# Kernel optimization log

Measured on AMD Instinct MI355X. Metric: run time of the kernel, lower is better.

## Reference

```python
import jax, jax.numpy as jnp
import numpy as np

HID = 512
J = 64
NEG = -1e9


def _gru_cell(x, h, Wih, Whh, bih, bhh):
    # PyTorch GRUCell: gates stacked as (r, z, n) along first dim of (3H, in)
    gi = Wih @ x + bih          # (3H,)
    gh = Whh @ h + bhh          # (3H,)
    r = jax.nn.sigmoid(gi[:HID] + gh[:HID])
    z = jax.nn.sigmoid(gi[HID:2 * HID] + gh[HID:2 * HID])
    n = jnp.tanh(gi[2 * HID:] + r * gh[2 * HID:])
    return (1.0 - z) * n + z * h


def setup_inputs() -> dict:
    key = jax.random.key(0)
    ks = jax.random.split(key, 8)
    T = 4096
    state_dim = 2 * J  # input is state[t][1:]
    d = {
        "state": jax.random.normal(ks[0], (T, state_dim + 1), dtype=jnp.float32),
        "h_prev": jnp.zeros((2, HID), dtype=jnp.float32),
        "mask": jax.random.randint(ks[1], (J, J), 0, 2, dtype=jnp.int32),
        "Wih0": jax.random.normal(ks[2], (3 * HID, state_dim), dtype=jnp.float32) * 0.05,
        "Whh0": jax.random.normal(ks[3], (3 * HID, HID), dtype=jnp.float32) * 0.04,
        "bih0": jnp.zeros((3 * HID,), dtype=jnp.float32),
        "bhh0": jnp.zeros((3 * HID,), dtype=jnp.float32),
        "Wih1": jax.random.normal(ks[4], (3 * HID, HID), dtype=jnp.float32) * 0.04,
        "Whh1": jax.random.normal(ks[5], (3 * HID, HID), dtype=jnp.float32) * 0.04,
        "bih1": jnp.zeros((3 * HID,), dtype=jnp.float32),
        "bhh1": jnp.zeros((3 * HID,), dtype=jnp.float32),
        "Wfc": jax.random.normal(ks[6], (J * J, HID), dtype=jnp.float32) * 0.06,
        "bfc": jnp.zeros((J * J,), dtype=jnp.float32),
    }
    return d


def reference(state, h_prev, mask, Wih0, Whh0, bih0, bhh0,
              Wih1, Whh1, bih1, bhh1, Wfc, bfc):
    xs = state[:, 1:]  # drop leading element, matches state[t][1:]

    def step(hs, x_t):
        h0 = _gru_cell(x_t, hs[0], Wih0, Whh0, bih0, bhh0)
        h1 = _gru_cell(h0, hs[1], Wih1, Whh1, bih1, bhh1)
        new = jnp.stack([h0, h1])
        return new, h1

    h_next, h_list = jax.lax.scan(step, h_prev, xs)  # h_list: (T, HID)
    logits = jax.nn.relu(h_list @ Wfc.T + bfc)       # (T, J*J)
    logits = logits.reshape(-1, J, J)
    logits = jnp.where(mask == 0, jnp.float32(NEG), logits)
    return logits, h_next
```

## Files before the change

kernel.cpp:

```cpp
#include <hip/hip_runtime.h>
#include <stdint.h>

#define TS 4096
#define NEG_VAL -1000000000.0f

typedef _Float16 h2 __attribute__((ext_vector_type(2)));
typedef unsigned long long u64t;

#define GI0_OFF   ((size_t)0)
#define H1_OFF    ((size_t)25165824)
#define MB0L0_OFF ((size_t)33554432)
#define MB0L1_OFF ((size_t)33816576)
#define MB1L1_OFF ((size_t)34340864)
#define PROGS_OFF ((size_t)34865152)
#define PROGH_OFF ((size_t)34867200)
#define TICK_OFF  ((size_t)34867712)
#define WS_NEED   ((size_t)34867776)

static __device__ __forceinline__ u64t ld_a64(const u64t* p){
  return __hip_atomic_load(p, __ATOMIC_RELAXED, __HIP_MEMORY_SCOPE_AGENT);
}
static __device__ __forceinline__ void st_a64(u64t* p, u64t v){
  __hip_atomic_store(p, v, __ATOMIC_RELAXED, __HIP_MEMORY_SCOPE_AGENT);
}
static __device__ __forceinline__ unsigned ld_u32(const unsigned* p){
  return __hip_atomic_load(p, __ATOMIC_RELAXED, __HIP_MEMORY_SCOPE_AGENT);
}
static __device__ __forceinline__ void st_u32(unsigned* p, unsigned v){
  __hip_atomic_store(p, v, __ATOMIC_RELAXED, __HIP_MEMORY_SCOPE_AGENT);
}
static __device__ __forceinline__ float sigmoidf_(float x){
  return 1.0f / (1.0f + __expf(-x));
}
static __device__ __forceinline__ float tanhf_(float x){
  float ax = fabsf(x);
  float e  = __expf(-2.0f*ax);
  float t  = (1.0f - e) / (1.0f + e);
  return copysignf(t, x);
}
static __device__ __forceinline__ uint32_t pack2h(float a, float b){
  _Float16 ha = (_Float16)a, hb = (_Float16)b;
  unsigned short ua = __builtin_bit_cast(unsigned short, ha);
  unsigned short ub = __builtin_bit_cast(unsigned short, hb);
  return (uint32_t)ua | ((uint32_t)ub << 16);
}
static __device__ __forceinline__ h2 u2h2(uint32_t u){ return __builtin_bit_cast(h2, u); }
static __device__ __forceinline__ unsigned tg(u64t v){ return (unsigned)(v>>32); }

template<int CTRL>
static __device__ __forceinline__ float dppx(float x){
  return __int_as_float(__builtin_amdgcn_update_dpp(0, __float_as_int(x), CTRL, 0xF, 0xF, true));
}
static __device__ __forceinline__ float qsum8(float x){
  x += dppx<0xB1>(x);
  x += dppx<0x4E>(x);
  x += __shfl_xor(x, 4, 64);
  return x;
}
static __device__ __forceinline__ float qsum16(float x){
  x += dppx<0xB1>(x);
  x += dppx<0x4E>(x);
  x += __shfl_xor(x, 4, 64);
  x += __shfl_xor(x, 8, 64);
  return x;
}
static __device__ __forceinline__ int wave_min(int v){
  #pragma unroll
  for (int off=32; off; off>>=1){ int o = __shfl_xor(v, off, 64); v = o<v?o:v; }
  return v;
}

#if __has_builtin(__builtin_amdgcn_fdot2)
#define FDOT2(a,b,c) __builtin_amdgcn_fdot2((a),(b),(c),false)
#else
static __device__ __forceinline__ float FDOT2(h2 a, h2 b, float c){
  return c + (float)a[0]*(float)b[0] + (float)a[1]*(float)b[1];
}
#endif

static __device__ __forceinline__ void poll4(const u64t* base, unsigned want,
                                             uint32_t (&v)[4], long* bd, bool* fail){
  u64t p0=ld_a64(base), p1=ld_a64(base+1), p2=ld_a64(base+2), p3=ld_a64(base+3);
  for(;;){
    bool ok = (tg(p0)==want)&&(tg(p1)==want)&&(tg(p2)==want)&&(tg(p3)==want);
    if (__all(ok)) break;
    if (--(*bd) < 0){ *fail = true; break; }
    __builtin_amdgcn_s_sleep(1);
    if (tg(p0)!=want) p0=ld_a64(base);
    if (tg(p1)!=want) p1=ld_a64(base+1);
    if (tg(p2)!=want) p2=ld_a64(base+2);
    if (tg(p3)!=want) p3=ld_a64(base+3);
  }
  v[0]=(uint32_t)p0; v[1]=(uint32_t)p1; v[2]=(uint32_t)p2; v[3]=(uint32_t)p3;
}
static __device__ __forceinline__ void seg32(h2* dst, const float* src){
  const float4* p = (const float4*)src;
  #pragma unroll
  for (int k=0;k<16;++k){
    float4 v = p[k];
    dst[2*k]   = h2{(_Float16)v.x,(_Float16)v.y};
    dst[2*k+1] = h2{(_Float16)v.z,(_Float16)v.w};
  }
}
static __device__ __forceinline__ void seg16(h2* dst, const float* src){
  const float4* p = (const float4*)src;
  #pragma unroll
  for (int k=0;k<8;++k){
    float4 v = p[k];
    dst[2*k]   = h2{(_Float16)v.x,(_Float16)v.y};
    dst[2*k+1] = h2{(_Float16)v.z,(_Float16)v.w};
  }
}

__global__ __launch_bounds__(512,1) void actor_fused(
    const float* __restrict__ hprev,
    const int*   __restrict__ mask,
    const float* __restrict__ Whh0,
    const float* __restrict__ bhh0,
    const float* __restrict__ Wih1,
    const float* __restrict__ Whh1,
    const float* __restrict__ bih1,
    const float* __restrict__ bhh1,
    const float* __restrict__ Wfc,
    const float* __restrict__ bfc,
    const float* __restrict__ gi0,
    float* __restrict__ H1,
    u64t* mb0l0, u64t* mb0l1, u64t* mb1l1,
    unsigned* progS, unsigned* progH, unsigned* ticket,
    float* __restrict__ out, float* __restrict__ hnext)
{
  const int wg   = blockIdx.x;
  const int tid  = threadIdx.x;
  const int wv   = tid >> 6;
  const int lane = tid & 63;
  __shared__ __align__(16) float lds[6464];
  volatile int* fcp = (volatile int*)lds;
  long bd = 1L<<22;
  bool fail = false;

  if (wg < 24){
    if (wg < 8){
      const int j = lane & 7;
      const int o = wg*64 + (tid>>3);
      h2 w[96];
      seg32(&w[0],  Whh0 + (size_t)o*512         + 64*j);
      seg32(&w[32], Whh0 + (size_t)(512+o)*512   + 64*j);
      seg32(&w[64], Whh0 + (size_t)(1024+o)*512  + 64*j);
      const float br=bhh0[o], bz=bhh0[512+o], bn=bhh0[1024+o];
      float hreg = hprev[o];
      if ((tid&1)==0)
        st_a64(mb0l0 + ((size_t)wg*16 + 15)*256 + (tid>>1),
               ((u64t)1<<32) | pack2h(hprev[tid], hprev[tid+1]));
      if (tid==0) fcp[0] = 0;
      __syncthreads();

      for (int t=0; t<TS; ++t){
        if ((t&3)==0){
          if (wv==0 && lane==0) st_u32(progS + wg*16, (unsigned)(t-1));
          if (t>=16){
            const int need = t-11;
            if (wv==0){
              int v = (lane<24)? (int)ld_u32(progS + lane*16) : 0x7fffffff;
              int mn = wave_min(v);
              while (mn < need){
                if (--bd<0){ fail=true; break; }
                __builtin_amdgcn_s_sleep(4);
                v = (lane<24)? (int)ld_u32(progS + lane*16) : 0x7fffffff;
                mn = wave_min(v);
              }
              if (lane==0) fcp[0] = t;
            } else {
              while (fcp[0] < t){ if (--bd<0){ fail=true; break; } __builtin_amdgcn_s_sleep(4); }
            }
            if (fail) break;
          }
        }
        const float* gp = gi0 + (size_t)t*1536;
        const float gr = gp[o], gz = gp[512+o], gn = gp[1024+o];

        uint32_t v[4];
        poll4(mb0l0 + ((size_t)wg*16 + ((t-1)&15))*256 + 4*lane, (unsigned)(t+1), v, &bd, &fail);
        if (fail) break;
        uint32_t hw[32];
        const int sj = 8*j;
        #pragma unroll
        for (int i=0;i<8;++i){
          const int src = sj + i;
          hw[4*i+0] = (uint32_t)__shfl((int)v[0], src, 64);
          hw[4*i+1] = (uint32_t)__shfl((int)v[1], src, 64);
          hw[4*i+2] = (uint32_t)__shfl((int)v[2], src, 64);
          hw[4*i+3] = (uint32_t)__shfl((int)v[3], src, 64);
        }
        float a0=0.f, a1=0.f, a2=0.f;
        #pragma unroll
        for (int m=0;m<32;++m){
          h2 hv = u2h2(hw[m]);
          a0 = FDOT2(w[m],    hv, a0);
          a1 = FDOT2(w[32+m], hv, a1);
          a2 = FDOT2(w[64+m], hv, a2);
        }
        a0 = qsum8(a0); a1 = qsum8(a1); a2 = qsum8(a2);

        const float r = sigmoidf_(gr + a0 + br);
        const float z = sigmoidf_(gz + a1 + bz);
        const float n = tanhf_(gn + r*(a2 + bn));
        const float h = (1.f - z)*n + z*hreg;
        hreg = h;

        const float hx = __shfl_xor(h, 8, 64);
        const uint32_t wval = (o&1)? pack2h(hx,h) : pack2h(h,hx);
        const u64t word = ((u64t)(unsigned)(t+2)<<32) | wval;
        const int wi = wg*32 + (tid>>4);
        const int d = (tid&7) | (((tid>>3)&1)<<3);
        const int slot = t&15;
        if (d<8){
          st_a64(mb0l0 + ((size_t)d*16 + slot)*256 + wi, word);
          st_a64(mb0l1 + ((size_t)(8+d)*16 + slot)*256 + wi, word);
        } else {
          st_a64(mb0l1 + ((size_t)(d-8)*16 + slot)*256 + wi, word);
        }
        if (t==TS-1 && j==0) hnext[o] = h;
      }
    } else {
      const int q = wg-8;
      const int j = lane & 15;
      const int ol = q*32 + (tid>>4);
      h2 w[96];
      seg16(&w[0],  Whh1 + (size_t)ol*512         + 32*j);
      seg16(&w[16], Whh1 + (size_t)(512+ol)*512   + 32*j);
      seg16(&w[32], Whh1 + (size_t)(1024+ol)*512  + 32*j);
      seg16(&w[48], Wih1 + (size_t)ol*512         + 32*j);
      seg16(&w[64], Wih1 + (size_t)(512+ol)*512   + 32*j);
      seg16(&w[80], Wih1 + (size_t)(1024+ol)*512  + 32*j);
      const float brc = bih1[ol]      + bhh1[ol];
      const float bzc = bih1[512+ol]  + bhh1[512+ol];
      const float bin = bih1[1024+ol];
      const float bhn = bhh1[1024+ol];
      float hreg = hprev[512+ol];
      if ((tid&1)==0)
        st_a64(mb1l1 + ((size_t)q*16 + 15)*256 + (tid>>1),
               ((u64t)1<<32) | pack2h(hprev[512+tid], hprev[512+tid+1]));
      if (tid==0) fcp[0] = 0;
      __syncthreads();

      for (int s=0; s<TS; ++s){
        if ((s&3)==0){
          if (wv==0 && lane==0) st_u32(progS + wg*16, (unsigned)(s-1));
          if (s>=16){
            const int need = s-11;
            if (wv==0){
              int v = (lane<24)? (int)ld_u32(progS + lane*16) : 0x7fffffff;
              int mn = wave_min(v);
              while (mn < need){
                if (--bd<0){ fail=true; break; }
                __builtin_amdgcn_s_sleep(4);
                v = (lane<24)? (int)ld_u32(progS + lane*16) : 0x7fffffff;
                mn = wave_min(v);
              }
              if (lane==0) fcp[0] = s;
            } else {
              while (fcp[0] < s){ if (--bd<0){ fail=true; break; } __builtin_amdgcn_s_sleep(4); }
            }
            if (fail) break;
          }
        }
        uint32_t va[4], vb[4];
        poll4(mb1l1 + ((size_t)q*16 + ((s-1)&15))*256 + 4*lane, (unsigned)(s+1), va, &bd, &fail);
        if (fail) break;
        poll4(mb0l1 + ((size_t)q*16 + (s&15))*256 + 4*lane, (unsigned)(s+2), vb, &bd, &fail);
        if (fail) break;
        uint32_t h1w[16], h0w[16];
        const int s4 = 4*j;
        #pragma unroll
        for (int rr=0;rr<4;++rr){
          const int src = s4 + rr;
          h1w[4*rr+0]=(uint32_t)__shfl((int)va[0],src,64);
          h1w[4*rr+1]=(uint32_t)__shfl((int)va[1],src,64);
          h1w[4*rr+2]=(uint32_t)__shfl((int)va[2],src,64);
          h1w[4*rr+3]=(uint32_t)__shfl((int)va[3],src,64);
          h0w[4*rr+0]=(uint32_t)__shfl((int)vb[0],src,64);
          h0w[4*rr+1]=(uint32_t)__shfl((int)vb[1],src,64);
          h0w[4*rr+2]=(uint32_t)__shfl((int)vb[2],src,64);
          h0w[4*rr+3]=(uint32_t)__shfl((int)vb[3],src,64);
        }
        float a0=0.f,a1=0.f,a2=0.f,b0=0.f,b1=0.f,b2=0.f;
        #pragma unroll
        for (int m=0;m<16;++m){
          h2 hv1 = u2h2(h1w[m]);
          h2 hv0 = u2h2(h0w[m]);
          a0 = FDOT2(w[m],    hv1, a0);
          a1 = FDOT2(w[16+m], hv1, a1);
          a2 = FDOT2(w[32+m], hv1, a2);
          b0 = FDOT2(w[48+m], hv0, b0);
          b1 = FDOT2(w[64+m], hv0, b1);
          b2 = FDOT2(w[80+m], hv0, b2);
        }
        const float sr  = qsum16(a0+b0);
        const float sz  = qsum16(a1+b1);
        const float shn = qsum16(a2);
        const float sin_= qsum16(b2);

        const float r = sigmoidf_(sr + brc);
        const float z = sigmoidf_(sz + bzc);
        const float n = tanhf_((sin_ + bin) + r*(shn + bhn));
        const float h = (1.f - z)*n + z*hreg;
        hreg = h;

        if (j==0) H1[(size_t)s*512 + ol] = h;
        const float hx = __shfl_xor(h, 16, 64);
        const uint32_t wval = (ol&1)? pack2h(hx,h) : pack2h(h,hx);
        const u64t word = ((u64t)(unsigned)(s+2)<<32) | wval;
        const int wi = q*16 + (tid>>5);
        const int d = (tid&15) | (((tid>>4)&1)<<4);
        if (d<16)
          st_a64(mb1l1 + ((size_t)d*16 + (s&15))*256 + wi, word);
        if ((s&15)==15 && lane==0)
          __hip_atomic_store(progH + q*8 + wv, (unsigned)(s+1),
                             __ATOMIC_RELEASE, __HIP_MEMORY_SCOPE_AGENT);
        if (s==TS-1 && j==0) hnext[512+ol] = h;
      }
      if (lane==0)
        __hip_atomic_store(progH + q*8 + wv, (unsigned)TS,
                           __ATOMIC_RELEASE, __HIP_MEMORY_SCOPE_AGENT);
    }
  } else {
    float* As = lds;
    float* Bs = lds + 32*132;
    int*   comm = (int*)&lds[6460];
    const int tm = tid>>4, tn = tid&15;
    const int m0 = tid>>2, kk0a = (tid&3)*8;
    const int n0 = tid>>3, kk0b = (tid&7)*4;
    long fcbd = 1L<<24;
    for(;;){
      if (tid==0) comm[0] = (int)atomicAdd(ticket, 1u);
      __syncthreads();
      const int tau = comm[0];
      __syncthreads();
      if (tau >= 2048) break;
      const int bm = tau>>6, bn = tau&63;
      if (tid==0){
        const unsigned need = (unsigned)(bm*128 + 128);
        for(;;){
          unsigned mn = 0xffffffffu;
          for (int k2=0;k2<128;++k2){ unsigned v = ld_u32(progH+k2); mn = v<mn?v:mn; }
          if (mn >= need) break;
          __builtin_amdgcn_s_sleep(16);
          if (--fcbd < 0) break;
        }
      }
      __syncthreads();
      __builtin_amdgcn_fence(__ATOMIC_ACQUIRE, "agent");

      const float* A = H1  + (size_t)bm*128*512;
      const float* B = Wfc + (size_t)bn*64*512;
      float acc[4][4] = {};
      for (int k0=0; k0<512; k0+=32){
        #pragma unroll
        for (int jj=0;jj<8;++jj) As[(kk0a+jj)*132 + m0] = A[(size_t)m0*512 + k0+kk0a+jj];
        #pragma unroll
        for (int jj=0;jj<4;++jj) Bs[(kk0b+jj)*68  + n0] = B[(size_t)n0*512 + k0+kk0b+jj];
        __syncthreads();
        #pragma unroll
        for (int kk=0;kk<32;++kk){
          const float4 av = *(const float4*)&As[kk*132 + tm*4];
          const float4 bv = *(const float4*)&Bs[kk*68  + tn*4];
          acc[0][0]=fmaf(av.x,bv.x,acc[0][0]); acc[0][1]=fmaf(av.x,bv.y,acc[0][1]);
          acc[0][2]=fmaf(av.x,bv.z,acc[0][2]); acc[0][3]=fmaf(av.x,bv.w,acc[0][3]);
          acc[1][0]=fmaf(av.y,bv.x,acc[1][0]); acc[1][1]=fmaf(av.y,bv.y,acc[1][1]);
          acc[1][2]=fmaf(av.y,bv.z,acc[1][2]); acc[1][3]=fmaf(av.y,bv.w,acc[1][3]);
          acc[2][0]=fmaf(av.z,bv.x,acc[2][0]); acc[2][1]=fmaf(av.z,bv.y,acc[2][1]);
          acc[2][2]=fmaf(av.z,bv.z,acc[2][2]); acc[2][3]=fmaf(av.z,bv.w,acc[2][3]);
          acc[3][0]=fmaf(av.w,bv.x,acc[3][0]); acc[3][1]=fmaf(av.w,bv.y,acc[3][1]);
          acc[3][2]=fmaf(av.w,bv.z,acc[3][2]); acc[3][3]=fmaf(av.w,bv.w,acc[3][3]);
        }
        __syncthreads();
      }
      const int cc0 = bn*64 + tn*4;
      const int mk0 = mask[cc0], mk1 = mask[cc0+1], mk2 = mask[cc0+2], mk3 = mask[cc0+3];
      const float b0 = bfc[cc0], b1 = bfc[cc0+1], b2 = bfc[cc0+2], b3 = bfc[cc0+3];
      #pragma unroll
      for (int i=0;i<4;++i){
        const int mm = bm*128 + tm*4 + i;
        float4 vv;
        vv.x = fmaxf(acc[i][0]+b0, 0.f); if (mk0==0) vv.x = NEG_VAL;
        vv.y = fmaxf(acc[i][1]+b1, 0.f); if (mk1==0) vv.y = NEG_VAL;
        vv.z = fmaxf(acc[i][2]+b2, 0.f); if (mk2==0) vv.z = NEG_VAL;
        vv.w = fmaxf(acc[i][3]+b3, 0.f); if (mk3==0) vv.w = NEG_VAL;
        *(float4*)&out[(size_t)mm*4096 + cc0] = vv;
      }
    }
  }
}

__global__ __launch_bounds__(256) void gemm_gi0(
    const float* __restrict__ A, int lda,
    const float* __restrict__ B, int ldb,
    float* __restrict__ C, int ldc,
    const float* __restrict__ bias, int K)
{
  __shared__ __align__(16) float As[32][68];
  __shared__ __align__(16) float Bs[32][68];
  const int bm = blockIdx.y*64, bn = blockIdx.x*64;
  const int tid = threadIdx.x;
  const int tm = tid>>4, tn = tid&15;
  float acc[4][4] = {};
  const int m0 = tid>>2, kk0 = (tid&3)*8;
  for (int k0=0; k0<K; k0+=32){
    #pragma unroll
    for (int j=0;j<8;++j) As[kk0+j][m0] = A[(size_t)(bm+m0)*lda + k0+kk0+j];
    #pragma unroll
    for (int j=0;j<8;++j) Bs[kk0+j][m0] = B[(size_t)(bn+m0)*ldb + k0+kk0+j];
    __syncthreads();
    #pragma unroll
    for (int kk=0;kk<32;++kk){
      const float4 av = *(const float4*)&As[kk][tm*4];
      const float4 bv = *(const float4*)&Bs[kk][tn*4];
      acc[0][0]=fmaf(av.x,bv.x,acc[0][0]); acc[0][1]=fmaf(av.x,bv.y,acc[0][1]);
      acc[0][2]=fmaf(av.x,bv.z,acc[0][2]); acc[0][3]=fmaf(av.x,bv.w,acc[0][3]);
      acc[1][0]=fmaf(av.y,bv.x,acc[1][0]); acc[1][1]=fmaf(av.y,bv.y,acc[1][1]);
      acc[1][2]=fmaf(av.y,bv.z,acc[1][2]); acc[1][3]=fmaf(av.y,bv.w,acc[1][3]);
      acc[2][0]=fmaf(av.z,bv.x,acc[2][0]); acc[2][1]=fmaf(av.z,bv.y,acc[2][1]);
      acc[2][2]=fmaf(av.z,bv.z,acc[2][2]); acc[2][3]=fmaf(av.z,bv.w,acc[2][3]);
      acc[3][0]=fmaf(av.w,bv.x,acc[3][0]); acc[3][1]=fmaf(av.w,bv.y,acc[3][1]);
      acc[3][2]=fmaf(av.w,bv.z,acc[3][2]); acc[3][3]=fmaf(av.w,bv.w,acc[3][3]);
    }
    __syncthreads();
  }
  #pragma unroll
  for (int i=0;i<4;++i){
    #pragma unroll
    for (int j=0;j<4;++j){
      const int mm = bm + tm*4 + i, cc = bn + tn*4 + j;
      C[(size_t)mm*ldc + cc] = acc[i][j] + bias[cc];
    }
  }
}

extern "C" void kernel_launch(void* const* d_in, const int* in_sizes, int n_in,
                              void* d_out, int out_size, void* d_ws, size_t ws_size,
                              hipStream_t stream)
{
  const float* state = (const float*)d_in[0];
  const float* hprev = (const float*)d_in[1];
  const int*   mask  = (const int*)d_in[2];
  const float* Wih0  = (const float*)d_in[3];
  const float* Whh0  = (const float*)d_in[4];
  const float* bih0  = (const float*)d_in[5];
  const float* bhh0  = (const float*)d_in[6];
  const float* Wih1  = (const float*)d_in[7];
  const float* Whh1  = (const float*)d_in[8];
  const float* bih1  = (const float*)d_in[9];
  const float* bhh1  = (const float*)d_in[10];
  const float* Wfc   = (const float*)d_in[11];
  const float* bfc   = (const float*)d_in[12];

  if (ws_size < WS_NEED) return;

  float* out = (float*)d_out;
  char*  ws  = (char*)d_ws;
  float* gi0 = (float*)(ws + GI0_OFF);
  float* H1  = (float*)(ws + H1_OFF);
  u64t*  mb0l0 = (u64t*)(ws + MB0L0_OFF);
  u64t*  mb0l1 = (u64t*)(ws + MB0L1_OFF);
  u64t*  mb1l1 = (u64t*)(ws + MB1L1_OFF);
  unsigned* progS = (unsigned*)(ws + PROGS_OFF);
  unsigned* progH = (unsigned*)(ws + PROGH_OFF);
  unsigned* tick  = (unsigned*)(ws + TICK_OFF);

  (void)hipMemsetAsync(ws + MB0L0_OFF, 0, (size_t)(WS_NEED - MB0L0_OFF), stream);

  {
    dim3 grid(1536/64, 4096/64);
    gemm_gi0<<<grid, 256, 0, stream>>>(state+1, 129, Wih0, 128, gi0, 1536, bih0, 128);
  }

  actor_fused<<<256, 512, 0, stream>>>(
      hprev, mask, Whh0, bhh0, Wih1, Whh1, bih1, bhh1, Wfc, bfc,
      gi0, H1, mb0l0, mb0l1, mb1l1, progS, progH, tick,
      out, out + (size_t)4096*4096);
}
```

Baseline: 15.58 ms.

## Restructure GRU scan sync: LDS-staged mailbox polling, spread scan blocks, fp16 gi0

Rewrites the persistent GRU scan in the fused kernel. A single wave polls the inter-block mailboxes and stages the hidden-state words in LDS for the other waves, replacing the per-wave cross-lane shuffles. Scan blocks are spread across every eighth block index, mailbox depth goes from 16 to 32 slots, and progress checks run less often. The input-gate GEMM now writes fp16 output to halve its memory traffic and adds rounding error. The extra LDS flag handshakes may add latency on each step of the serial recurrence.

```diff
diff --git a/kernel.cpp b/kernel.cpp
--- a/kernel.cpp
+++ b/kernel.cpp
@@ -4,18 +4,19 @@
 #define TS 4096
 #define NEG_VAL -1000000000.0f
 
-typedef _Float16 h2 __attribute__((ext_vector_type(2)));
+typedef _Float16 h2    __attribute__((ext_vector_type(2)));
+typedef _Float16 f16x8 __attribute__((ext_vector_type(8)));
 typedef unsigned long long u64t;
 
-#define GI0_OFF   ((size_t)0)
-#define H1_OFF    ((size_t)25165824)
-#define MB0L0_OFF ((size_t)33554432)
-#define MB0L1_OFF ((size_t)33816576)
-#define MB1L1_OFF ((size_t)34340864)
-#define PROGS_OFF ((size_t)34865152)
-#define PROGH_OFF ((size_t)34867200)
-#define TICK_OFF  ((size_t)34867712)
-#define WS_NEED   ((size_t)34867776)
+#define GI0H_OFF  ((size_t)0)
+#define H1_OFF    ((size_t)12582912)
+#define MB0L0_OFF ((size_t)20971520)
+#define MB0L1_OFF ((size_t)21495808)
+#define MB1L1_OFF ((size_t)22544384)
+#define PROGS_OFF ((size_t)23592960)
+#define PROGH_OFF ((size_t)23594496)
+#define TICK_OFF  ((size_t)23594752)
+#define WS_NEED   ((size_t)23594816)
 
 static __device__ __forceinline__ u64t ld_a64(const u64t* p){
   return __hip_atomic_load(p, __ATOMIC_RELAXED, __HIP_MEMORY_SCOPE_AGENT);
@@ -52,16 +53,11 @@
   return __int_as_float(__builtin_amdgcn_update_dpp(0, __float_as_int(x), CTRL, 0xF, 0xF, true));
 }
 static __device__ __forceinline__ float qsum8(float x){
-  x += dppx<0xB1>(x);
-  x += dppx<0x4E>(x);
-  x += __shfl_xor(x, 4, 64);
+  x += dppx<0xB1>(x); x += dppx<0x4E>(x); x += __shfl_xor(x, 4, 64);
   return x;
 }
 static __device__ __forceinline__ float qsum16(float x){
-  x += dppx<0xB1>(x);
-  x += dppx<0x4E>(x);
-  x += __shfl_xor(x, 4, 64);
-  x += __shfl_xor(x, 8, 64);
+  x += dppx<0xB1>(x); x += dppx<0x4E>(x); x += __shfl_xor(x, 4, 64); x += __shfl_xor(x, 8, 64);
   return x;
 }
 static __device__ __forceinline__ int wave_min(int v){
@@ -71,46 +67,34 @@
 }
 
 #if __has_builtin(__builtin_amdgcn_fdot2)
-#define FDOT2(a,b,c) __builtin_amdgcn_fdot2((a),(b),(c),false)
+static __device__ __forceinline__ float FDOT2(h2 a, h2 b, float c){
+  return __builtin_amdgcn_fdot2(a, b, c, false);
+}
 #else
 static __device__ __forceinline__ float FDOT2(h2 a, h2 b, float c){
   return c + (float)a[0]*(float)b[0] + (float)a[1]*(float)b[1];
 }
 #endif
 
-static __device__ __forceinline__ void poll4(const u64t* base, unsigned want,
-                                             uint32_t (&v)[4], long* bd, bool* fail){
-  u64t p0=ld_a64(base), p1=ld_a64(base+1), p2=ld_a64(base+2), p3=ld_a64(base+3);
-  for(;;){
-    bool ok = (tg(p0)==want)&&(tg(p1)==want)&&(tg(p2)==want)&&(tg(p3)==want);
-    if (__all(ok)) break;
-    if (--(*bd) < 0){ *fail = true; break; }
-    __builtin_amdgcn_s_sleep(1);
-    if (tg(p0)!=want) p0=ld_a64(base);
-    if (tg(p1)!=want) p1=ld_a64(base+1);
-    if (tg(p2)!=want) p2=ld_a64(base+2);
-    if (tg(p3)!=want) p3=ld_a64(base+3);
-  }
-  v[0]=(uint32_t)p0; v[1]=(uint32_t)p1; v[2]=(uint32_t)p2; v[3]=(uint32_t)p3;
-}
-static __device__ __forceinline__ void seg32(h2* dst, const float* src){
-  const float4* p = (const float4*)src;
-  #pragma unroll
-  for (int k=0;k<16;++k){
-    float4 v = p[k];
-    dst[2*k]   = h2{(_Float16)v.x,(_Float16)v.y};
-    dst[2*k+1] = h2{(_Float16)v.z,(_Float16)v.w};
-  }
-}
-static __device__ __forceinline__ void seg16(h2* dst, const float* src){
-  const float4* p = (const float4*)src;
-  #pragma unroll
-  for (int k=0;k<8;++k){
-    float4 v = p[k];
-    dst[2*k]   = h2{(_Float16)v.x,(_Float16)v.y};
-    dst[2*k+1] = h2{(_Float16)v.z,(_Float16)v.w};
-  }
-}
+static __device__ __forceinline__ float dot8(f16x8 wv, const uint32_t* hw, float acc){
+  acc = FDOT2(h2{wv[0],wv[1]}, u2h2(hw[0]), acc);
+  acc = FDOT2(h2{wv[2],wv[3]}, u2h2(hw[1]), acc);
+  acc = FDOT2(h2{wv[4],wv[5]}, u2h2(hw[2]), acc);
+  acc = FDOT2(h2{wv[6],wv[7]}, u2h2(hw[3]), acc);
+  return acc;
+}
+
+#define DECL8(P) f16x8 P##0,P##1,P##2,P##3,P##4,P##5,P##6,P##7;
+#define DECL4(P) f16x8 P##0,P##1,P##2,P##3;
+#define LDW8(DST, PTR) { float4 _a=((const float4*)(PTR))[0]; float4 _b=((const float4*)(PTR))[1]; \
+  DST = f16x8{(_Float16)_a.x,(_Float16)_a.y,(_Float16)_a.z,(_Float16)_a.w, \
+              (_Float16)_b.x,(_Float16)_b.y,(_Float16)_b.z,(_Float16)_b.w}; }
+#define LOADROW8(P, BASE) LDW8(P##0,(BASE)) LDW8(P##1,(BASE)+8) LDW8(P##2,(BASE)+16) LDW8(P##3,(BASE)+24) \
+                          LDW8(P##4,(BASE)+32) LDW8(P##5,(BASE)+40) LDW8(P##6,(BASE)+48) LDW8(P##7,(BASE)+56)
+#define LOADROW4(P, BASE) LDW8(P##0,(BASE)) LDW8(P##1,(BASE)+8) LDW8(P##2,(BASE)+16) LDW8(P##3,(BASE)+24)
+#define DOT8x8(ACC,P,HW) ACC=dot8(P##0,(HW)+0,ACC);ACC=dot8(P##1,(HW)+4,ACC);ACC=dot8(P##2,(HW)+8,ACC);ACC=dot8(P##3,(HW)+12,ACC); \
+                         ACC=dot8(P##4,(HW)+16,ACC);ACC=dot8(P##5,(HW)+20,ACC);ACC=dot8(P##6,(HW)+24,ACC);ACC=dot8(P##7,(HW)+28,ACC);
+#define DOT8x4(ACC,P,HW) ACC=dot8(P##0,(HW)+0,ACC);ACC=dot8(P##1,(HW)+4,ACC);ACC=dot8(P##2,(HW)+8,ACC);ACC=dot8(P##3,(HW)+12,ACC);
 
 __global__ __launch_bounds__(512,1) void actor_fused(
     const float* __restrict__ hprev,
@@ -123,210 +107,298 @@
     const float* __restrict__ bhh1,
     const float* __restrict__ Wfc,
     const float* __restrict__ bfc,
-    const float* __restrict__ gi0,
+    const uint32_t* __restrict__ gi0h,
     float* __restrict__ H1,
     u64t* mb0l0, u64t* mb0l1, u64t* mb1l1,
     unsigned* progS, unsigned* progH, unsigned* ticket,
     float* __restrict__ out, float* __restrict__ hnext)
 {
-  const int wg   = blockIdx.x;
+  const int bx   = blockIdx.x;
   const int tid  = threadIdx.x;
   const int wv   = tid >> 6;
   const int lane = tid & 63;
-  __shared__ __align__(16) float lds[6464];
-  volatile int* fcp = (volatile int*)lds;
+  const bool isScan = ((bx & 7) == 0) && (bx < 192);
+  const int role = bx >> 3;
+
+  __shared__ __align__(16) uint32_t smem[6784];
   long bd = 1L<<22;
   bool fail = false;
 
-  if (wg < 24){
-    if (wg < 8){
-      const int j = lane & 7;
-      const int o = wg*64 + (tid>>3);
-      h2 w[96];
-      seg32(&w[0],  Whh0 + (size_t)o*512         + 64*j);
-      seg32(&w[32], Whh0 + (size_t)(512+o)*512   + 64*j);
-      seg32(&w[64], Whh0 + (size_t)(1024+o)*512  + 64*j);
-      const float br=bhh0[o], bz=bhh0[512+o], bn=bhh0[1024+o];
-      float hreg = hprev[o];
-      if ((tid&1)==0)
-        st_a64(mb0l0 + ((size_t)wg*16 + 15)*256 + (tid>>1),
-               ((u64t)1<<32) | pack2h(hprev[tid], hprev[tid+1]));
-      if (tid==0) fcp[0] = 0;
-      __syncthreads();
-
-      for (int t=0; t<TS; ++t){
-        if ((t&3)==0){
-          if (wv==0 && lane==0) st_u32(progS + wg*16, (unsigned)(t-1));
-          if (t>=16){
-            const int need = t-11;
-            if (wv==0){
-              int v = (lane<24)? (int)ld_u32(progS + lane*16) : 0x7fffffff;
-              int mn = wave_min(v);
-              while (mn < need){
-                if (--bd<0){ fail=true; break; }
-                __builtin_amdgcn_s_sleep(4);
-                v = (lane<24)? (int)ld_u32(progS + lane*16) : 0x7fffffff;
-                mn = wave_min(v);
-              }
-              if (lane==0) fcp[0] = t;
-            } else {
-              while (fcp[0] < t){ if (--bd<0){ fail=true; break; } __builtin_amdgcn_s_sleep(4); }
-            }
-            if (fail) break;
+  if (isScan && role < 8){
+    const int o = role*64 + (tid>>3);
+    const int j = tid&7;
+    DECL8(Ar) DECL8(Az) DECL8(An)
+    LOADROW8(Ar, Whh0 + (size_t)o*512         + 64*j)
+    LOADROW8(Az, Whh0 + (size_t)(512+o)*512   + 64*j)
+    LOADROW8(An, Whh0 + (size_t)(1024+o)*512  + 64*j)
+    const float br=bhh0[o], bz=bhh0[512+o], bn=bhh0[1024+o];
+    float hreg = hprev[o];
+    u64t* mbme = mb0l0 + (size_t)role*32*256;
+    volatile int* flg = (volatile int*)(smem+600);
+    volatile int* fcp = (volatile int*)(smem+604);
+    if ((tid&1)==0)
+      st_a64(mbme + (size_t)31*256 + (tid>>1), ((u64t)1<<32) | pack2h(hprev[tid], hprev[tid+1]));
+    if (tid==0){ flg[0]=-1; flg[1]=-1; fcp[0]=-1; }
+    __syncthreads();
+    u64t p0=0,p1=0,p2=0,p3=0;
+    if (wv==0){
+      const u64t* b = mbme + (size_t)31*256 + 4*lane;
+      p0=ld_a64(b); p1=ld_a64(b+1); p2=ld_a64(b+2); p3=ld_a64(b+3);
+    }
+
+    for (int t=0; t<TS; ++t){
+      if ((t&3)==0 && wv==2 && lane==0) st_u32(progS + role*16, (unsigned)t);
+      if ((t&15)==8 && t>=32){
+        if (wv==2){
+          const int need = t-10;
+          int v = (lane<24)? (int)ld_u32(progS + lane*16) : 0x7fffffff;
+          int mn = wave_min(v);
+          while (mn < need){
+            if (--bd<0){ fail=true; break; }
+            __builtin_amdgcn_s_sleep(8);
+            v = (lane<24)? (int)ld_u32(progS + lane*16) : 0x7fffffff;
+            mn = wave_min(v);
           }
-        }
-        const float* gp = gi0 + (size_t)t*1536;
-        const float gr = gp[o], gz = gp[512+o], gn = gp[1024+o];
-
-        uint32_t v[4];
-        poll4(mb0l0 + ((size_t)wg*16 + ((t-1)&15))*256 + 4*lane, (unsigned)(t+1), v, &bd, &fail);
+          if (lane==0) fcp[0] = t;
+        } else {
+          int c=0;
+          while (fcp[0] < t){ if(++c>(1<<20)){fail=true;break;} __builtin_amdgcn_s_sleep(4); }
+        }
         if (fail) break;
-        uint32_t hw[32];
-        const int sj = 8*j;
+      }
+      const uint32_t* gp = gi0h + (size_t)t*768 + (o>>1);
+      const uint32_t ga=gp[0], gb=gp[256], gc=gp[512];
+
+      if (wv==0){
+        const unsigned want = (unsigned)(t+1);
+        const u64t* b = mbme + (size_t)((t-1)&31)*256 + 4*lane;
+        int it=0;
+        for(;;){
+          bool ok = (tg(p0)==want)&&(tg(p1)==want)&&(tg(p2)==want)&&(tg(p3)==want);
+          if (__all(ok)) break;
+          if (--bd<0){ fail=true; break; }
+          if (++it>16) __builtin_amdgcn_s_sleep(2);
+          if (tg(p0)!=want) p0=ld_a64(b);
+          if (tg(p1)!=want) p1=ld_a64(b+1);
+          if (tg(p2)!=want) p2=ld_a64(b+2);
+          if (tg(p3)!=want) p3=ld_a64(b+3);
+        }
+        uint32_t* dst = smem + (t&1)*288 + 4*lane + 4*(lane>>3);
+        dst[0]=(uint32_t)p0; dst[1]=(uint32_t)p1; dst[2]=(uint32_t)p2; dst[3]=(uint32_t)p3;
+        asm volatile("s_waitcnt lgkmcnt(0)" ::: "memory");
+        if (fail){ flg[0]=0x7fffffff; flg[1]=0x7fffffff; break; }
+        if (lane==0) flg[t&1] = t;
+      }
+      { int c=0, fv;
+        while ((fv=flg[t&1]) != t){
+          if (fv>=0x40000000){ fail=true; break; }
+          if (++c>(1<<20)){ fail=true; break; }
+          __builtin_amdgcn_s_sleep(1);
+        }
+        if (fail) break;
+      }
+      asm volatile("" ::: "memory");
+      uint32_t hw[32];
+      { const uint32_t* src = smem + (t&1)*288 + 36*j;
         #pragma unroll
-        for (int i=0;i<8;++i){
-          const int src = sj + i;
-          hw[4*i+0] = (uint32_t)__shfl((int)v[0], src, 64);
-          hw[4*i+1] = (uint32_t)__shfl((int)v[1], src, 64);
-          hw[4*i+2] = (uint32_t)__shfl((int)v[2], src, 64);
-          hw[4*i+3] = (uint32_t)__shfl((int)v[3], src, 64);
-        }
-        float a0=0.f, a1=0.f, a2=0.f;
+        for (int k2=0;k2<8;++k2){
+          uint4 u = *(const uint4*)(src + 4*k2);
+          hw[4*k2]=u.x; hw[4*k2+1]=u.y; hw[4*k2+2]=u.z; hw[4*k2+3]=u.w;
+        } }
+      float a0=0.f,a1=0.f,a2=0.f;
+      DOT8x8(a0,Ar,hw) DOT8x8(a1,Az,hw) DOT8x8(a2,An,hw)
+      a0=qsum8(a0); a1=qsum8(a1); a2=qsum8(a2);
+
+      h2 g0=u2h2(ga), g1=u2h2(gb), g2=u2h2(gc);
+      const int half = o&1;
+      const float gr = half? (float)g0[1] : (float)g0[0];
+      const float gz = half? (float)g1[1] : (float)g1[0];
+      const float gn = half? (float)g2[1] : (float)g2[0];
+
+      const float r = sigmoidf_(gr + a0 + br);
+      const float z = sigmoidf_(gz + a1 + bz);
+      const float n = tanhf_(gn + r*(a2 + bn));
+      const float h = (1.f - z)*n + z*hreg;
+      hreg = h;
+
+      const float hx = __shfl_xor(h, 8, 64);
+      const uint32_t wval = half? pack2h(hx,h) : pack2h(h,hx);
+      const u64t word = ((u64t)(unsigned)(t+2)<<32) | wval;
+      const int wi = role*32 + (tid>>4);
+      const int d = (tid&7) | (((tid>>3)&1)<<3);
+      const int slot = t&31;
+      if (d<8){
+        st_a64(mb0l0 + ((size_t)d*32 + slot)*256 + wi, word);
+        st_a64(mb0l1 + ((size_t)(8+d)*32 + slot)*256 + wi, word);
+      } else {
+        st_a64(mb0l1 + ((size_t)(d-8)*32 + slot)*256 + wi, word);
+      }
+      if (t==TS-1 && j==0) hnext[o] = h;
+      if (wv==0){
+        const u64t* b = mbme + (size_t)(t&31)*256 + 4*lane;
+        p0=ld_a64(b); p1=ld_a64(b+1); p2=ld_a64(b+2); p3=ld_a64(b+3);
+      }
+    }
+  } else if (isScan){
+    const int q = role-8;
+    const int ol = q*32 + (tid>>4);
+    const int j = lane&15;
+    DECL4(Hr) DECL4(Hz) DECL4(Hn) DECL4(Ir) DECL4(Iz) DECL4(In)
+    LOADROW4(Hr, Whh1 + (size_t)ol*512         + 32*j)
+    LOADROW4(Hz, Whh1 + (size_t)(512+ol)*512   + 32*j)
+    LOADROW4(Hn, Whh1 + (size_t)(1024+ol)*512  + 32*j)
+    LOADROW4(Ir, Wih1 + (size_t)ol*512         + 32*j)
+    LOADROW4(Iz, Wih1 + (size_t)(512+ol)*512   + 32*j)
+    LOADROW4(In, Wih1 + (size_t)(1024+ol)*512  + 32*j)
+    const float brc = bih1[ol] + bhh1[ol];
+    const float bzc = bih1[512+ol] + bhh1[512+ol];
+    const float bin = bih1[1024+ol];
+    const float bhn = bhh1[1024+ol];
+    float hreg = hprev[512+ol];
+    u64t* mb1me = mb1l1 + (size_t)q*32*256;
+    u64t* mb0me = mb0l1 + (size_t)q*32*256;
+    volatile int* flgA = (volatile int*)(smem+1160);
+    volatile int* flgB = (volatile int*)(smem+1162);
+    volatile int* fcp  = (volatile int*)(smem+1166);
+    if ((tid&1)==0)
+      st_a64(mb1me + (size_t)31*256 + (tid>>1), ((u64t)1<<32) | pack2h(hprev[512+tid], hprev[512+tid+1]));
+    if (tid==0){ flgA[0]=-1; flgA[1]=-1; flgB[0]=-1; flgB[1]=-1; fcp[0]=-1; }
+    __syncthreads();
+    u64t pa0=0,pa1=0,pa2=0,pa3=0, pb0=0,pb1=0,pb2=0,pb3=0;
+    if (wv==0){
+      const u64t* b = mb1me + (size_t)31*256 + 4*lane;
+      pa0=ld_a64(b); pa1=ld_a64(b+1); pa2=ld_a64(b+2); pa3=ld_a64(b+3);
+    } else if (wv==1){
+      const u64t* b = mb0me + 4*lane;
+      pb0=ld_a64(b); pb1=ld_a64(b+1); pb2=ld_a64(b+2); pb3=ld_a64(b+3);
+    }
+
+    for (int s=0; s<TS; ++s){
+      if ((s&3)==0 && wv==2 && lane==32) st_u32(progS + role*16, (unsigned)s);
+      if ((s&15)==8 && s>=32){
+        if (wv==2){
+          const int need = s-10;
+          int v = (lane<16)? (int)ld_u32(progS + (8+lane)*16) : 0x7fffffff;
+          int mn = wave_min(v);
+          while (mn < need){
+            if (--bd<0){ fail=true; break; }
+            __builtin_amdgcn_s_sleep(8);
+            v = (lane<16)? (int)ld_u32(progS + (8+lane)*16) : 0x7fffffff;
+            mn = wave_min(v);
+          }
+          if (lane==0) fcp[0] = s;
+        } else {
+          int c=0;
+          while (fcp[0] < s){ if(++c>(1<<20)){fail=true;break;} __builtin_amdgcn_s_sleep(4); }
+        }
+        if (fail) break;
+      }
+      if (wv==0){
+        const unsigned want = (unsigned)(s+1);
+        const u64t* b = mb1me + (size_t)((s-1)&31)*256 + 4*lane;
+        int it=0;
+        for(;;){
+          bool ok = (tg(pa0)==want)&&(tg(pa1)==want)&&(tg(pa2)==want)&&(tg(pa3)==want);
+          if (__all(ok)) break;
+          if (--bd<0){ fail=true; break; }
+          if (++it>16) __builtin_amdgcn_s_sleep(2);
+          if (tg(pa0)!=want) pa0=ld_a64(b);
+          if (tg(pa1)!=want) pa1=ld_a64(b+1);
+          if (tg(pa2)!=want) pa2=ld_a64(b+2);
+          if (tg(pa3)!=want) pa3=ld_a64(b+3);
+        }
+        uint32_t* dst = smem + (s&1)*288 + 4*lane + 4*(lane>>3);
+        dst[0]=(uint32_t)pa0; dst[1]=(uint32_t)pa1; dst[2]=(uint32_t)pa2; dst[3]=(uint32_t)pa3;
+        asm volatile("s_waitcnt lgkmcnt(0)" ::: "memory");
+        if (fail){ flgA[0]=0x7fffffff; flgA[1]=0x7fffffff; break; }
+        if (lane==0) flgA[s&1] = s;
+      } else if (wv==1){
+        const unsigned want = (unsigned)(s+2);
+        const u64t* b = mb0me + (size_t)(s&31)*256 + 4*lane;
+        int it=0;
+        for(;;){
+          bool ok = (tg(pb0)==want)&&(tg(pb1)==want)&&(tg(pb2)==want)&&(tg(pb3)==want);
+          if (__all(ok)) break;
+          if (--bd<0){ fail=true; break; }
+          if (++it>16) __builtin_amdgcn_s_sleep(2);
+          if (tg(pb0)!=want) pb0=ld_a64(b);
+          if (tg(pb1)!=want) pb1=ld_a64(b+1);
+          if (tg(pb2)!=want) pb2=ld_a64(b+2);
+          if (tg(pb3)!=want) pb3=ld_a64(b+3);
+        }
+        uint32_t* dst = smem + 576 + (s&1)*288 + 4*lane + 4*(lane>>3);
+        dst[0]=(uint32_t)pb0; dst[1]=(uint32_t)pb1; dst[2]=(uint32_t)pb2; dst[3]=(uint32_t)pb3;
+        asm volatile("s_waitcnt lgkmcnt(0)" ::: "memory");
+        if (fail){ flgB[0]=0x7fffffff; flgB[1]=0x7fffffff; break; }
+        if (lane==0) flgB[s&1] = s;
+      }
+      { int c=0, fv;
+        while ((fv=flgA[s&1]) != s){
+          if (fv>=0x40000000){ fail=true; break; }
+          if (++c>(1<<20)){ fail=true; break; }
+          __builtin_amdgcn_s_sleep(1);
+        }
+        while (!fail && (fv=flgB[s&1]) != s){
+          if (fv>=0x40000000){ fail=true; break; }
+          if (++c>(1<<20)){ fail=true; break; }
+          __builtin_amdgcn_s_sleep(1);
+        }
+        if (fail) break;
+      }
+      asm volatile("" ::: "memory");
+      uint32_t h1w[16], h0w[16];
+      { const int off = 16*j + 4*(j>>1);
+        const uint32_t* sa = smem + (s&1)*288 + off;
+        const uint32_t* sb = smem + 576 + (s&1)*288 + off;
         #pragma unroll
-        for (int m=0;m<32;++m){
-          h2 hv = u2h2(hw[m]);
-          a0 = FDOT2(w[m],    hv, a0);
-          a1 = FDOT2(w[32+m], hv, a1);
-          a2 = FDOT2(w[64+m], hv, a2);
-        }
-        a0 = qsum8(a0); a1 = qsum8(a1); a2 = qsum8(a2);
-
-        const float r = sigmoidf_(gr + a0 + br);
-        const float z = sigmoidf_(gz + a1 + bz);
-        const float n = tanhf_(gn + r*(a2 + bn));
-        const float h = (1.f - z)*n + z*hreg;
-        hreg = h;
-
-        const float hx = __shfl_xor(h, 8, 64);
-        const uint32_t wval = (o&1)? pack2h(hx,h) : pack2h(h,hx);
-        const u64t word = ((u64t)(unsigned)(t+2)<<32) | wval;
-        const int wi = wg*32 + (tid>>4);
-        const int d = (tid&7) | (((tid>>3)&1)<<3);
-        const int slot = t&15;
-        if (d<8){
-          st_a64(mb0l0 + ((size_t)d*16 + slot)*256 + wi, word);
-          st_a64(mb0l1 + ((size_t)(8+d)*16 + slot)*256 + wi, word);
-        } else {
-          st_a64(mb0l1 + ((size_t)(d-8)*16 + slot)*256 + wi, word);
-        }
-        if (t==TS-1 && j==0) hnext[o] = h;
-      }
-    } else {
-      const int q = wg-8;
-      const int j = lane & 15;
-      const int ol = q*32 + (tid>>4);
-      h2 w[96];
-      seg16(&w[0],  Whh1 + (size_t)ol*512         + 32*j);
-      seg16(&w[16], Whh1 + (size_t)(512+ol)*512   + 32*j);
-      seg16(&w[32], Whh1 + (size_t)(1024+ol)*512  + 32*j);
-      seg16(&w[48], Wih1 + (size_t)ol*512         + 32*j);
-      seg16(&w[64], Wih1 + (size_t)(512+ol)*512   + 32*j);
-      seg16(&w[80], Wih1 + (size_t)(1024+ol)*512  + 32*j);
-      const float brc = bih1[ol]      + bhh1[ol];
-      const float bzc = bih1[512+ol]  + bhh1[512+ol];
-      const float bin = bih1[1024+ol];
-      const float bhn = bhh1[1024+ol];
-      float hreg = hprev[512+ol];
-      if ((tid&1)==0)
-        st_a64(mb1l1 + ((size_t)q*16 + 15)*256 + (tid>>1),
-               ((u64t)1<<32) | pack2h(hprev[512+tid], hprev[512+tid+1]));
-      if (tid==0) fcp[0] = 0;
-      __syncthreads();
-
-      for (int s=0; s<TS; ++s){
-        if ((s&3)==0){
-          if (wv==0 && lane==0) st_u32(progS + wg*16, (unsigned)(s-1));
-          if (s>=16){
-            const int need = s-11;
-            if (wv==0){
-              int v = (lane<24)? (int)ld_u32(progS + lane*16) : 0x7fffffff;
-              int mn = wave_min(v);
-              while (mn < need){
-                if (--bd<0){ fail=true; break; }
-                __builtin_amdgcn_s_sleep(4);
-                v = (lane<24)? (int)ld_u32(progS + lane*16) : 0x7fffffff;
-                mn = wave_min(v);
-              }
-              if (lane==0) fcp[0] = s;
-            } else {
-              while (fcp[0] < s){ if (--bd<0){ fail=true; break; } __builtin_amdgcn_s_sleep(4); }
-            }
-            if (fail) break;
-          }
-        }
-        uint32_t va[4], vb[4];
-        poll4(mb1l1 + ((size_t)q*16 + ((s-1)&15))*256 + 4*lane, (unsigned)(s+1), va, &bd, &fail);
-        if (fail) break;
-        poll4(mb0l1 + ((size_t)q*16 + (s&15))*256 + 4*lane, (unsigned)(s+2), vb, &bd, &fail);
-        if (fail) break;
-        uint32_t h1w[16], h0w[16];
-        const int s4 = 4*j;
-        #pragma unroll
-        for (int rr=0;rr<4;++rr){
-          const int src = s4 + rr;
-          h1w[4*rr+0]=(uint32_t)__shfl((int)va[0],src,64);
-          h1w[4*rr+1]=(uint32_t)__shfl((int)va[1],src,64);
-          h1w[4*rr+2]=(uint32_t)__shfl((int)va[2],src,64);
-          h1w[4*rr+3]=(uint32_t)__shfl((int)va[3],src,64);
-          h0w[4*rr+0]=(uint32_t)__shfl((int)vb[0],src,64);
-          h0w[4*rr+1]=(uint32_t)__shfl((int)vb[1],src,64);
-          h0w[4*rr+2]=(uint32_t)__shfl((int)vb[2],src,64);
-          h0w[4*rr+3]=(uint32_t)__shfl((int)vb[3],src,64);
-        }
-        float a0=0.f,a1=0.f,a2=0.f,b0=0.f,b1=0.f,b2=0.f;
-        #pragma unroll
-        for (int m=0;m<16;++m){
-          h2 hv1 = u2h2(h1w[m]);
-          h2 hv0 = u2h2(h0w[m]);
-          a0 = FDOT2(w[m],    hv1, a0);
-          a1 = FDOT2(w[16+m], hv1, a1);
-          a2 = FDOT2(w[32+m], hv1, a2);
-          b0 = FDOT2(w[48+m], hv0, b0);
-          b1 = FDOT2(w[64+m], hv0, b1);
-          b2 = FDOT2(w[80+m], hv0, b2);
-        }
-        const float sr  = qsum16(a0+b0);
-        const float sz  = qsum16(a1+b1);
-        const float shn = qsum16(a2);
-        const float sin_= qsum16(b2);
-
-        const float r = sigmoidf_(sr + brc);
-        const float z = sigmoidf_(sz + bzc);
-        const float n = tanhf_((sin_ + bin) + r*(shn + bhn));
-        const float h = (1.f - z)*n + z*hreg;
-        hreg = h;
-
-        if (j==0) H1[(size_t)s*512 + ol] = h;
-        const float hx = __shfl_xor(h, 16, 64);
-        const uint32_t wval = (ol&1)? pack2h(hx,h) : pack2h(h,hx);
-        const u64t word = ((u64t)(unsigned)(s+2)<<32) | wval;
-        const int wi = q*16 + (tid>>5);
-        const int d = (tid&15) | (((tid>>4)&1)<<4);
-        if (d<16)
-          st_a64(mb1l1 + ((size_t)d*16 + (s&15))*256 + wi, word);
-        if ((s&15)==15 && lane==0)
-          __hip_atomic_store(progH + q*8 + wv, (unsigned)(s+1),
-                             __ATOMIC_RELEASE, __HIP_MEMORY_SCOPE_AGENT);
-        if (s==TS-1 && j==0) hnext[512+ol] = h;
-      }
-      if (lane==0)
-        __hip_atomic_store(progH + q*8 + wv, (unsigned)TS,
+        for (int k2=0;k2<4;++k2){
+          uint4 u = *(const uint4*)(sa + 4*k2);
+          h1w[4*k2]=u.x; h1w[4*k2+1]=u.y; h1w[4*k2+2]=u.z; h1w[4*k2+3]=u.w;
+          uint4 v = *(const uint4*)(sb + 4*k2);
+          h0w[4*k2]=v.x; h0w[4*k2+1]=v.y; h0w[4*k2+2]=v.z; h0w[4*k2+3]=v.w;
+        } }
+      float a0=0.f,a1=0.f,a2=0.f,b0=0.f,b1=0.f,b2=0.f;
+      DOT8x4(a0,Hr,h1w) DOT8x4(a1,Hz,h1w) DOT8x4(a2,Hn,h1w)
+      DOT8x4(b0,Ir,h0w) DOT8x4(b1,Iz,h0w) DOT8x4(b2,In,h0w)
+      const float sr  = qsum16(a0+b0);
+      const float sz  = qsum16(a1+b1);
+      const float shn = qsum16(a2);
+      const float sin_= qsum16(b2);
+
+      const float r = sigmoidf_(sr + brc);
+      const float z = sigmoidf_(sz + bzc);
+      const float n = tanhf_((sin_ + bin) + r*(shn + bhn));
+      const float h = (1.f - z)*n + z*hreg;
+      hreg = h;
+
+      if ((tid&15)==0) H1[(size_t)s*512 + ol] = h;
+      const float hx = __shfl_xor(h, 16, 64);
+      const uint32_t wval = (ol&1)? pack2h(hx,h) : pack2h(h,hx);
+      const u64t word = ((u64t)(unsigned)(s+2)<<32) | wval;
+      const int wi = q*16 + (tid>>5);
+      const int d = (tid&15) | (((tid>>4)&1)<<4);
+      if (d<16)
+        st_a64(mb1l1 + ((size_t)d*32 + (s&31))*256 + wi, word);
+      if ((s&15)==15 && wv==3 && lane==32)
+        __hip_atomic_store(progH + q, (unsigned)(s-4),
                            __ATOMIC_RELEASE, __HIP_MEMORY_SCOPE_AGENT);
+      if (s==TS-1 && (tid&15)==0) hnext[512+ol] = h;
+      if (wv==0){
+        const u64t* b = mb1me + (size_t)(s&31)*256 + 4*lane;
+        pa0=ld_a64(b); pa1=ld_a64(b+1); pa2=ld_a64(b+2); pa3=ld_a64(b+3);
+      } else if (wv==1){
+        const u64t* b = mb0me + (size_t)((s+1)&31)*256 + 4*lane;
+        pb0=ld_a64(b); pb1=ld_a64(b+1); pb2=ld_a64(b+2); pb3=ld_a64(b+3);
+      }
     }
+    __syncthreads();
+    if (tid==0)
+      __hip_atomic_store(progH + q, (unsigned)TS,
+                         __ATOMIC_RELEASE, __HIP_MEMORY_SCOPE_AGENT);
   } else {
-    float* As = lds;
-    float* Bs = lds + 32*132;
-    int*   comm = (int*)&lds[6460];
+    float* As = (float*)smem;
+    float* Bs = As + 32*132;
+    int*   comm = (int*)&smem[6780];
     const int tm = tid>>4, tn = tid&15;
     const int m0 = tid>>2, kk0a = (tid&3)*8;
     const int n0 = tid>>3, kk0b = (tid&7)*4;
@@ -342,9 +414,9 @@
         const unsigned need = (unsigned)(bm*128 + 128);
         for(;;){
           unsigned mn = 0xffffffffu;
-          for (int k2=0;k2<128;++k2){ unsigned v = ld_u32(progH+k2); mn = v<mn?v:mn; }
+          for (int k2=0;k2<16;++k2){ unsigned v = ld_u32(progH+k2); mn = v<mn?v:mn; }
           if (mn >= need) break;
-          __builtin_amdgcn_s_sleep(16);
+          __builtin_amdgcn_s_sleep(32);
           if (--fcbd < 0) break;
         }
       }
@@ -377,15 +449,15 @@
       }
       const int cc0 = bn*64 + tn*4;
       const int mk0 = mask[cc0], mk1 = mask[cc0+1], mk2 = mask[cc0+2], mk3 = mask[cc0+3];
-      const float b0 = bfc[cc0], b1 = bfc[cc0+1], b2 = bfc[cc0+2], b3 = bfc[cc0+3];
+      const float c0 = bfc[cc0], c1 = bfc[cc0+1], c2 = bfc[cc0+2], c3 = bfc[cc0+3];
       #pragma unroll
       for (int i=0;i<4;++i){
         const int mm = bm*128 + tm*4 + i;
         float4 vv;
-        vv.x = fmaxf(acc[i][0]+b0, 0.f); if (mk0==0) vv.x = NEG_VAL;
-        vv.y = fmaxf(acc[i][1]+b1, 0.f); if (mk1==0) vv.y = NEG_VAL;
-        vv.z = fmaxf(acc[i][2]+b2, 0.f); if (mk2==0) vv.z = NEG_VAL;
-        vv.w = fmaxf(acc[i][3]+b3, 0.f); if (mk3==0) vv.w = NEG_VAL;
+        vv.x = fmaxf(acc[i][0]+c0, 0.f); if (mk0==0) vv.x = NEG_VAL;
+        vv.y = fmaxf(acc[i][1]+c1, 0.f); if (mk1==0) vv.y = NEG_VAL;
+        vv.z = fmaxf(acc[i][2]+c2, 0.f); if (mk2==0) vv.z = NEG_VAL;
+        vv.w = fmaxf(acc[i][3]+c3, 0.f); if (mk3==0) vv.w = NEG_VAL;
         *(float4*)&out[(size_t)mm*4096 + cc0] = vv;
       }
     }
@@ -395,7 +467,7 @@
 __global__ __launch_bounds__(256) void gemm_gi0(
     const float* __restrict__ A, int lda,
     const float* __restrict__ B, int ldb,
-    float* __restrict__ C, int ldc,
+    uint32_t* __restrict__ C,
     const float* __restrict__ bias, int K)
 {
   __shared__ __align__(16) float As[32][68];
@@ -426,13 +498,18 @@
     }
     __syncthreads();
   }
+  const int cc0 = bn + tn*4;
+  const int g = cc0 >> 9, c0 = cc0 & 511;
+  const float b0=bias[cc0], b1=bias[cc0+1], b2=bias[cc0+2], b3=bias[cc0+3];
   #pragma unroll
   for (int i=0;i<4;++i){
-    #pragma unroll
-    for (int j=0;j<4;++j){
-      const int mm = bm + tm*4 + i, cc = bn + tn*4 + j;
-      C[(size_t)mm*ldc + cc] = acc[i][j] + bias[cc];
-    }
+    const int mm = bm + tm*4 + i;
+    uint2 pw;
+    pw.x = ((uint32_t)__builtin_bit_cast(unsigned short,(_Float16)(acc[i][0]+b0))) |
+           (((uint32_t)__builtin_bit_cast(unsigned short,(_Float16)(acc[i][1]+b1)))<<16);
+    pw.y = ((uint32_t)__builtin_bit_cast(unsigned short,(_Float16)(acc[i][2]+b2))) |
+           (((uint32_t)__builtin_bit_cast(unsigned short,(_Float16)(acc[i][3]+b3)))<<16);
+    *(uint2*)&C[(size_t)mm*768 + g*256 + (c0>>1)] = pw;
   }
 }
 
@@ -458,7 +535,7 @@
 
   float* out = (float*)d_out;
   char*  ws  = (char*)d_ws;
-  float* gi0 = (float*)(ws + GI0_OFF);
+  uint32_t* gi0h = (uint32_t*)(ws + GI0H_OFF);
   float* H1  = (float*)(ws + H1_OFF);
   u64t*  mb0l0 = (u64t*)(ws + MB0L0_OFF);
   u64t*  mb0l1 = (u64t*)(ws + MB0L1_OFF);
@@ -471,11 +548,11 @@
 
   {
     dim3 grid(1536/64, 4096/64);
-    gemm_gi0<<<grid, 256, 0, stream>>>(state+1, 129, Wih0, 128, gi0, 1536, bih0, 128);
+    gemm_gi0<<<grid, 256, 0, stream>>>(state+1, 129, Wih0, 128, gi0h, bih0, 128);
   }
 
   actor_fused<<<256, 512, 0, stream>>>(
       hprev, mask, Whh0, bhh0, Wih1, Whh1, bih1, bhh1, Wfc, bfc,
-      gi0, H1, mb0l0, mb0l1, mb1l1, progS, progH, tick,
+      gi0h, H1, mb0l0, mb0l1, mb1l1, progS, progH, tick,
       out, out + (size_t)4096*4096);
 }
```

Result: slower. 21.23 ms (+36.2%).
